# Kernel optimization log

Measured on AMD Instinct MI355X. Metric: run time of the kernel, lower is better.

The kernel has to match this reference:

```python
import jax, jax.numpy as jnp
import numpy as np

DIM = 2048
DIM_SEQ = 2048
DIM_OUT = DIM // 2
LN_EPS = 1e-5


def setup_inputs() -> dict:
    key = jax.random.key(0)
    k1, k2 = jax.random.split(key)
    x = jax.random.normal(k1, (8, DIM_SEQ, DIM), dtype=jnp.float32)
    init_eps = 0.001 / DIM_SEQ
    # Conv1d(dim_seq, dim_seq, 1) weight -> [seq, seq] seq-mixing matrix
    proj_w = jax.random.uniform(k2, (DIM_SEQ, DIM_SEQ), minval=-init_eps, maxval=init_eps, dtype=jnp.float32)
    proj_b = jnp.ones((DIM_SEQ,), dtype=jnp.float32)
    ln_scale = jnp.ones((DIM_OUT,), dtype=jnp.float32)
    ln_bias = jnp.zeros((DIM_OUT,), dtype=jnp.float32)
    return {"x": x, "proj_w": proj_w, "proj_b": proj_b, "ln_scale": ln_scale, "ln_bias": ln_bias}


def reference(x, proj_w, proj_b, ln_scale, ln_bias):
    # chunk into residual and gate halves along feature dim
    res, gate = jnp.split(x, 2, axis=-1)  # each [b, s, d/2]
    # LayerNorm over last dim of gate
    mu = jnp.mean(gate, axis=-1, keepdims=True)
    var = jnp.mean(jnp.square(gate - mu), axis=-1, keepdims=True)
    gate = (gate - mu) * jax.lax.rsqrt(var + LN_EPS) * ln_scale + ln_bias
    # Conv1d kernel=1 over seq axis == seq-mixing matmul: [s,t] x [b,t,d] -> [b,s,d]
    gate = jnp.einsum('st,btd->bsd', proj_w, gate) + proj_b[None, :, None]
    # act = Identity; gated residual multiply
    return gate * res
```

## Files before the change

### kernel.cpp

```cpp
#include <hip/hip_runtime.h>

typedef __attribute__((ext_vector_type(8))) short short8;
typedef __attribute__((ext_vector_type(4))) float floatx4;

__device__ __forceinline__ unsigned short f2bf(float f) {
    unsigned int u = __builtin_bit_cast(unsigned int, f);
    u += 0x7fffu + ((u >> 16) & 1u);
    return (unsigned short)(u >> 16);
}

__device__ __forceinline__ void async16(unsigned short* lds, const unsigned short* g) {
    __builtin_amdgcn_global_load_lds(
        (__attribute__((address_space(1))) void*)(g),
        (__attribute__((address_space(3))) void*)(lds),
        16, 0, 0);
}

#define DIM      2048
#define DSEQ     2048
#define DOUT     1024
#define NBATCH   8
#define NKB      (DSEQ / 32)

__global__ __launch_bounds__(256) void cast_w_kernel(const float* __restrict__ w,
                                                     unsigned short* __restrict__ o) {
    int i = (blockIdx.x * 256 + threadIdx.x) * 4;
    int s = i >> 11;
    int t = i & 2047;
    float4 v = *(const float4*)(w + i);
    unsigned int lo = (unsigned int)f2bf(v.x) | ((unsigned int)f2bf(v.y) << 16);
    unsigned int hi = (unsigned int)f2bf(v.z) | ((unsigned int)f2bf(v.w) << 16);
    unsigned short* dst = o + (((size_t)(t >> 5)) * DSEQ + s) * 32 + (t & 31);
    *(uint2*)dst = make_uint2(lo, hi);
}

__global__ __launch_bounds__(256) void ln_t_kernel(const float* __restrict__ X,
                                                   const float* __restrict__ lns,
                                                   const float* __restrict__ lnb,
                                                   unsigned short* __restrict__ Gt) {
    const int tid  = threadIdx.x;
    const int wave = tid >> 6;
    const int lane = tid & 63;
    const int t0   = blockIdx.x * 32;
    const int b    = blockIdx.y;

    __shared__ unsigned short lt[32][1028];

    float4 sc[4], bi[4];
    #pragma unroll
    for (int c = 0; c < 4; ++c) {
        sc[c] = *(const float4*)(lns + c * 256 + lane * 4);
        bi[c] = *(const float4*)(lnb + c * 256 + lane * 4);
    }

    #pragma unroll 1
    for (int i = 0; i < 8; ++i) {
        const int r = wave * 8 + i;
        const float* xr = X + ((size_t)(b * DSEQ + t0 + r)) * DIM + DOUT;
        float4 v[4];
        float s = 0.f, ss = 0.f;
        #pragma unroll
        for (int c = 0; c < 4; ++c) {
            v[c] = *(const float4*)(xr + c * 256 + lane * 4);
            s  += v[c].x + v[c].y + v[c].z + v[c].w;
            ss += v[c].x * v[c].x + v[c].y * v[c].y + v[c].z * v[c].z + v[c].w * v[c].w;
        }
        #pragma unroll
        for (int off = 32; off > 0; off >>= 1) {
            s  += __shfl_xor(s,  off, 64);
            ss += __shfl_xor(ss, off, 64);
        }
        const float mu  = s * (1.f / 1024.f);
        const float var = ss * (1.f / 1024.f) - mu * mu;
        const float inv = rsqrtf(var + 1e-5f);
        #pragma unroll
        for (int c = 0; c < 4; ++c) {
            const int d = c * 256 + lane * 4;
            float y0 = (v[c].x - mu) * inv * sc[c].x + bi[c].x;
            float y1 = (v[c].y - mu) * inv * sc[c].y + bi[c].y;
            float y2 = (v[c].z - mu) * inv * sc[c].z + bi[c].z;
            float y3 = (v[c].w - mu) * inv * sc[c].w + bi[c].w;
            unsigned int lo = (unsigned int)f2bf(y0) | ((unsigned int)f2bf(y1) << 16);
            unsigned int hi = (unsigned int)f2bf(y2) | ((unsigned int)f2bf(y3) << 16);
            *(uint2*)&lt[r][d] = make_uint2(lo, hi);
        }
    }
    __syncthreads();

    #pragma unroll
    for (int it = 0; it < 4; ++it) {
        const int d = it * 256 + tid;
        unsigned int u[16];
        #pragma unroll
        for (int j = 0; j < 16; ++j)
            u[j] = (unsigned int)lt[2 * j][d] | ((unsigned int)lt[2 * j + 1][d] << 16);
        uint4* dst = (uint4*)(Gt + (((size_t)b * NKB + (t0 >> 5)) * DOUT + d) * 32);
        dst[0] = make_uint4(u[0],  u[1],  u[2],  u[3]);
        dst[1] = make_uint4(u[4],  u[5],  u[6],  u[7]);
        dst[2] = make_uint4(u[8],  u[9],  u[10], u[11]);
        dst[3] = make_uint4(u[12], u[13], u[14], u[15]);
    }
}

#define BM 128
#define BN 128
#define BK 64

__global__ __launch_bounds__(256) void gemm_sgu(const unsigned short* __restrict__ Wt,
                                                const unsigned short* __restrict__ Gt,
                                                const float* __restrict__ X,
                                                const float* __restrict__ Pb,
                                                float* __restrict__ Out) {
    const int tid = threadIdx.x;
    const int s0  = blockIdx.x * BM;
    const int d0  = blockIdx.y * BN;
    const int b   = blockIdx.z;

    __shared__ unsigned short As[BM * 64];
    __shared__ unsigned short Bs[BN * 64];

    const int wave = tid >> 6;
    const int lane = tid & 63;
    const int wr   = wave >> 1;
    const int wc   = wave & 1;
    const int ln15 = lane & 15;
    const int q    = lane >> 4;

    int ldsOff[4], srcA[4], srcB[4];
    #pragma unroll
    for (int j = 0; j < 4; ++j) {
        const int c   = tid + j * 256;
        const int r   = c >> 3;
        const int kc  = (c & 7) ^ (r & 7);
        const int u   = kc >> 2;
        const int cc  = kc & 3;
        ldsOff[j] = c * 8;
        srcA[j]   = (u * DSEQ + s0 + r) * 32 + cc * 8;
        srcB[j]   = (u * DOUT + d0 + r) * 32 + cc * 8;
    }
    int aOff[2][4], bOff[2][4];
    #pragma unroll
    for (int u = 0; u < 2; ++u)
        #pragma unroll
        for (int i = 0; i < 4; ++i) {
            const int ra = wr * 64 + i * 16 + ln15;
            const int rb = wc * 64 + i * 16 + ln15;
            aOff[u][i] = ra * 64 + (((u * 4 + q) ^ (ra & 7)) * 8);
            bOff[u][i] = rb * 64 + (((u * 4 + q) ^ (rb & 7)) * 8);
        }

    floatx4 acc[4][4] = {};

    const unsigned short* gB = Gt + (size_t)b * NKB * DOUT * 32;

    for (int kb = 0; kb < NKB; kb += 2) {
        const unsigned short* aBase = Wt + (size_t)kb * DSEQ * 32;
        const unsigned short* bBase = gB + (size_t)kb * DOUT * 32;
        __syncthreads();
        #pragma unroll
        for (int j = 0; j < 4; ++j) {
            async16(&As[ldsOff[j]], aBase + srcA[j]);
            async16(&Bs[ldsOff[j]], bBase + srcB[j]);
        }
        __syncthreads();

        #pragma unroll
        for (int u = 0; u < 2; ++u) {
            short8 af[4], bf[4];
            #pragma unroll
            for (int i = 0; i < 4; ++i) af[i] = *(const short8*)&As[aOff[u][i]];
            #pragma unroll
            for (int i = 0; i < 4; ++i) bf[i] = *(const short8*)&Bs[bOff[u][i]];
            #pragma unroll
            for (int i = 0; i < 4; ++i)
                #pragma unroll
                for (int j = 0; j < 4; ++j)
                    acc[i][j] = __builtin_amdgcn_mfma_f32_16x16x32_bf16(af[i], bf[j], acc[i][j], 0, 0, 0);
        }
    }

    #pragma unroll
    for (int i = 0; i < 4; ++i) {
        const int srow = s0 + wr * 64 + i * 16 + q * 4;
        const float4 pb4 = *(const float4*)(Pb + srow);
        #pragma unroll
        for (int j = 0; j < 4; ++j) {
            const int d = d0 + wc * 64 + j * 16 + ln15;
            #pragma unroll
            for (int r = 0; r < 4; ++r) {
                const int s = srow + r;
                const float g = acc[i][j][r] + ((const float*)&pb4)[r];
                const size_t xi = ((size_t)(b * DSEQ + s)) * DIM + d;
                const size_t oi = ((size_t)(b * DSEQ + s)) * DOUT + d;
                Out[oi] = g * X[xi];
            }
        }
    }
}

extern "C" void kernel_launch(void* const* d_in, const int* in_sizes, int n_in,
                              void* d_out, int out_size, void* d_ws, size_t ws_size,
                              hipStream_t stream) {
    const float* x    = (const float*)d_in[0];
    const float* pw   = (const float*)d_in[1];
    const float* pb   = (const float*)d_in[2];
    const float* lns  = (const float*)d_in[3];
    const float* lnb  = (const float*)d_in[4];
    float* out        = (float*)d_out;

    unsigned short* Wt = (unsigned short*)d_ws;
    unsigned short* Gt = (unsigned short*)((char*)d_ws + (size_t)DSEQ * DSEQ * 2);

    cast_w_kernel<<<dim3((DSEQ * DSEQ) / 1024), dim3(256), 0, stream>>>(pw, Wt);
    ln_t_kernel<<<dim3(DSEQ / 32, NBATCH), dim3(256), 0, stream>>>(x, lns, lnb, Gt);
    gemm_sgu<<<dim3(DSEQ / BM, DOUT / BN, NBATCH), dim3(256), 0, stream>>>(Wt, Gt, x, pb, out);
}
```

Measured before the change: 311.6 us.

## Double-buffer GEMM K tiles in LDS and vectorize epilogue through shared staging

The GEMM now uses a two-stage LDS ring with a K-step of 32. It issues the async global-to-LDS loads for the next tile before computing on the current one, so memory latency overlaps with MFMA work and only one barrier is needed per step. The epilogue stages accumulators through LDS so each thread reads X and writes Out with coalesced float4 accesses instead of scattered scalar ones. The cost is twice as many loop iterations and barriers, plus extra barriers in the epilogue.

```diff
diff --git a/kernel.cpp b/kernel.cpp
--- a/kernel.cpp
+++ b/kernel.cpp
@@ -104,7 +104,6 @@
 
 #define BM 128
 #define BN 128
-#define BK 64
 
 __global__ __launch_bounds__(256) void gemm_sgu(const unsigned short* __restrict__ Wt,
                                                 const unsigned short* __restrict__ Gt,
@@ -116,8 +115,7 @@
     const int d0  = blockIdx.y * BN;
     const int b   = blockIdx.z;
 
-    __shared__ unsigned short As[BM * 64];
-    __shared__ unsigned short Bs[BN * 64];
+    __shared__ __align__(16) unsigned char smem[32768];
 
     const int wave = tid >> 6;
     const int lane = tid & 63;
@@ -126,74 +124,99 @@
     const int ln15 = lane & 15;
     const int q    = lane >> 4;
 
-    int ldsOff[4], srcA[4], srcB[4];
-    #pragma unroll
-    for (int j = 0; j < 4; ++j) {
-        const int c   = tid + j * 256;
-        const int r   = c >> 3;
-        const int kc  = (c & 7) ^ (r & 7);
-        const int u   = kc >> 2;
-        const int cc  = kc & 3;
+    int ldsOff[2], srcA[2], srcB[2];
+    #pragma unroll
+    for (int j = 0; j < 2; ++j) {
+        const int c  = tid + j * 256;
+        const int r  = c >> 2;
+        const int kc = (c & 3) ^ (r & 3);
         ldsOff[j] = c * 8;
-        srcA[j]   = (u * DSEQ + s0 + r) * 32 + cc * 8;
-        srcB[j]   = (u * DOUT + d0 + r) * 32 + cc * 8;
-    }
-    int aOff[2][4], bOff[2][4];
-    #pragma unroll
-    for (int u = 0; u < 2; ++u)
-        #pragma unroll
-        for (int i = 0; i < 4; ++i) {
-            const int ra = wr * 64 + i * 16 + ln15;
-            const int rb = wc * 64 + i * 16 + ln15;
-            aOff[u][i] = ra * 64 + (((u * 4 + q) ^ (ra & 7)) * 8);
-            bOff[u][i] = rb * 64 + (((u * 4 + q) ^ (rb & 7)) * 8);
-        }
+        srcA[j]   = (s0 + r) * 32 + kc * 8;
+        srcB[j]   = (d0 + r) * 32 + kc * 8;
+    }
+    int aOff[4], bOff[4];
+    #pragma unroll
+    for (int i = 0; i < 4; ++i) {
+        const int ra = wr * 64 + i * 16 + ln15;
+        const int rb = wc * 64 + i * 16 + ln15;
+        aOff[i] = ra * 32 + ((q ^ (ra & 3)) * 8);
+        bOff[i] = rb * 32 + ((q ^ (rb & 3)) * 8);
+    }
 
     floatx4 acc[4][4] = {};
 
     const unsigned short* gB = Gt + (size_t)b * NKB * DOUT * 32;
 
-    for (int kb = 0; kb < NKB; kb += 2) {
-        const unsigned short* aBase = Wt + (size_t)kb * DSEQ * 32;
-        const unsigned short* bBase = gB + (size_t)kb * DOUT * 32;
-        __syncthreads();
-        #pragma unroll
-        for (int j = 0; j < 4; ++j) {
+    {
+        const unsigned short* aBase = Wt;
+        const unsigned short* bBase = gB;
+        unsigned short* As = (unsigned short*)(smem);
+        unsigned short* Bs = (unsigned short*)(smem + 8192);
+        #pragma unroll
+        for (int j = 0; j < 2; ++j) {
             async16(&As[ldsOff[j]], aBase + srcA[j]);
             async16(&Bs[ldsOff[j]], bBase + srcB[j]);
         }
+    }
+
+    for (int kb = 0; kb < NKB; ++kb) {
+        unsigned short* Asc = (unsigned short*)(smem + (kb & 1) * 16384);
+        unsigned short* Bsc = Asc + 8192 / 2;
         __syncthreads();
 
-        #pragma unroll
-        for (int u = 0; u < 2; ++u) {
-            short8 af[4], bf[4];
+        if (kb + 1 < NKB) {
+            const unsigned short* aBase = Wt + (size_t)(kb + 1) * DSEQ * 32;
+            const unsigned short* bBase = gB + (size_t)(kb + 1) * DOUT * 32;
+            unsigned short* Asn = (unsigned short*)(smem + ((kb + 1) & 1) * 16384);
+            unsigned short* Bsn = Asn + 8192 / 2;
             #pragma unroll
-            for (int i = 0; i < 4; ++i) af[i] = *(const short8*)&As[aOff[u][i]];
+            for (int j = 0; j < 2; ++j) {
+                async16(&Asn[ldsOff[j]], aBase + srcA[j]);
+                async16(&Bsn[ldsOff[j]], bBase + srcB[j]);
+            }
+        }
+
+        short8 af[4], bf[4];
+        #pragma unroll
+        for (int i = 0; i < 4; ++i) af[i] = *(const short8*)&Asc[aOff[i]];
+        #pragma unroll
+        for (int i = 0; i < 4; ++i) bf[i] = *(const short8*)&Bsc[bOff[i]];
+        #pragma unroll
+        for (int i = 0; i < 4; ++i)
             #pragma unroll
-            for (int i = 0; i < 4; ++i) bf[i] = *(const short8*)&Bs[bOff[u][i]];
+            for (int j = 0; j < 4; ++j)
+                acc[i][j] = __builtin_amdgcn_mfma_f32_16x16x32_bf16(af[i], bf[j], acc[i][j], 0, 0, 0);
+    }
+
+    float (*ep)[132] = (float (*)[132])smem;
+    const int gr  = tid >> 3;
+    const int seg = tid & 7;
+    #pragma unroll
+    for (int e = 0; e < 4; ++e) {
+        __syncthreads();
+        #pragma unroll
+        for (int j = 0; j < 4; ++j) {
+            const int C = wc * 64 + j * 16 + ln15;
             #pragma unroll
-            for (int i = 0; i < 4; ++i)
-                #pragma unroll
-                for (int j = 0; j < 4; ++j)
-                    acc[i][j] = __builtin_amdgcn_mfma_f32_16x16x32_bf16(af[i], bf[j], acc[i][j], 0, 0, 0);
-        }
-    }
-
-    #pragma unroll
-    for (int i = 0; i < 4; ++i) {
-        const int srow = s0 + wr * 64 + i * 16 + q * 4;
-        const float4 pb4 = *(const float4*)(Pb + srow);
-        #pragma unroll
-        for (int j = 0; j < 4; ++j) {
-            const int d = d0 + wc * 64 + j * 16 + ln15;
-            #pragma unroll
-            for (int r = 0; r < 4; ++r) {
-                const int s = srow + r;
-                const float g = acc[i][j][r] + ((const float*)&pb4)[r];
-                const size_t xi = ((size_t)(b * DSEQ + s)) * DIM + d;
-                const size_t oi = ((size_t)(b * DSEQ + s)) * DOUT + d;
-                Out[oi] = g * X[xi];
-            }
+            for (int r = 0; r < 4; ++r)
+                ep[wr * 16 + q * 4 + r][C] = acc[e][j][r];
+        }
+        __syncthreads();
+        const int s = s0 + (gr >> 4) * 64 + e * 16 + (gr & 15);
+        const int d = d0 + seg * 16;
+        const float pb = Pb[s];
+        const float* xr = X + ((size_t)(b * DSEQ + s)) * DIM + d;
+        float*       orow = Out + ((size_t)(b * DSEQ + s)) * DOUT + d;
+        #pragma unroll
+        for (int w = 0; w < 4; ++w) {
+            float4 c = *(const float4*)&ep[gr][seg * 16 + w * 4];
+            float4 x = *(const float4*)(xr + w * 4);
+            float4 o;
+            o.x = (c.x + pb) * x.x;
+            o.y = (c.y + pb) * x.y;
+            o.z = (c.z + pb) * x.z;
+            o.w = (c.w + pb) * x.w;
+            *(float4*)(orow + w * 4) = o;
         }
     }
 }
```

After: 310.7 us. No clear change (-0.3%).
